# Kernel tuning notes

Measured on AMD Instinct MI355X. Metric: run time of the kernel, lower is better.

Reference implementation:

```python
import jax, jax.numpy as jnp
import numpy as np

N_HEAD = 16
N_KV_HEAD = 4
HEAD_DIM = 128
N_EMBD = 2048
ROPE_BASE = 100000.0
EPS = 1e-6
MASK_VAL = -10000.0


def _rope_tables(t, dtype):
    half = HEAD_DIM // 2
    inv_freq = 1.0 / (ROPE_BASE ** (jnp.arange(half, dtype=jnp.float32) / half))
    freqs = jnp.arange(t, dtype=jnp.float32)[:, None] * inv_freq[None, :]  # [t, half]
    return jnp.cos(freqs).astype(dtype), jnp.sin(freqs).astype(dtype)


def _apply_rope(x, cos, sin):
    # x: [b, t, h, d]; cos/sin: [t, d//2]
    x1, x2 = jnp.split(x, 2, axis=-1)
    c = cos[None, :, None, :]
    s = sin[None, :, None, :]
    return jnp.concatenate([x1 * c + x2 * s, -x1 * s + x2 * c], axis=-1)


def _rms_norm(x):
    return x * jax.lax.rsqrt(jnp.mean(jnp.square(x), axis=-1, keepdims=True) + EPS)


def setup_inputs() -> dict:
    key = jax.random.key(0)
    ks = jax.random.split(key, 5)
    b, t = 2, 2048
    std = 0.02
    return {
        "x": jax.random.normal(ks[0], (b, t, N_EMBD), dtype=jnp.float32),
        "wq": jax.random.normal(ks[1], (N_EMBD, N_HEAD * HEAD_DIM), dtype=jnp.float32) * std,
        "wk": jax.random.normal(ks[2], (N_EMBD, N_KV_HEAD * HEAD_DIM), dtype=jnp.float32) * std,
        "wv": jax.random.normal(ks[3], (N_EMBD, N_KV_HEAD * HEAD_DIM), dtype=jnp.float32) * std,
        "wo": jax.random.normal(ks[4], (N_EMBD, N_EMBD), dtype=jnp.float32) * std,
    }


def reference(x, wq, wk, wv, wo):
    b, t, _ = x.shape
    group = N_HEAD // N_KV_HEAD

    q = (x @ wq).reshape(b, t, N_HEAD, HEAD_DIM)
    k = (x @ wk).reshape(b, t, N_KV_HEAD, HEAD_DIM)
    v = (x @ wv).reshape(b, t, N_KV_HEAD, HEAD_DIM)

    cos, sin = _rope_tables(t, x.dtype)
    q = _rms_norm(_apply_rope(q, cos, sin))
    k = _rms_norm(_apply_rope(k, cos, sin))

    # GQA expand: [b,t,kvh,d] -> [b,t,h,d]
    k = jnp.repeat(k, group, axis=2)
    v = jnp.repeat(v, group, axis=2)

    scale = jax.lax.rsqrt(jnp.asarray(HEAD_DIM, dtype=q.dtype))
    scores = jnp.einsum("bqhd,bkhd->bhqk", q, k) * scale  # [b,h,t,t]

    causal = jnp.tril(jnp.ones((t, t), dtype=bool))
    scores = jnp.where(causal[None, None, :, :], scores, jnp.asarray(MASK_VAL, scores.dtype))

    probs = jax.nn.softmax(scores.astype(jnp.float32), axis=-1).astype(scores.dtype)

    y = jnp.einsum("bhqk,bkhd->bqhd", probs, v).reshape(b, t, N_EMBD)
    return y @ wo
```

## Files before the change

kernel.cpp:

```cpp
#include <hip/hip_runtime.h>
#include <stdint.h>

typedef unsigned short u16;
typedef unsigned int   u32;
typedef float f32x4  __attribute__((ext_vector_type(4)));
typedef float f32x16 __attribute__((ext_vector_type(16)));
typedef short s16x8  __attribute__((ext_vector_type(8)));

#define T_SEQ 2048
#define NE    2048
#define NH    16
#define NKV   4
#define HD    128
#define QKVW  3072

__device__ __forceinline__ u16 f2bf(float f){
  u32 u = __float_as_uint(f);
  u32 r = u + 0x7FFFu + ((u >> 16) & 1u);
  return (u16)(r >> 16);
}
__device__ __forceinline__ float bf2f(u16 h){ return __uint_as_float(((u32)h) << 16); }

__device__ __forceinline__ u32 pkbf(float a, float b){
  u32 r; asm("v_cvt_pk_bf16_f32 %0, %1, %2" : "=v"(r) : "v"(a), "v"(b)); return r;
}

typedef __attribute__((address_space(3))) u32 lds_u32;
typedef __attribute__((address_space(1))) u32 glb_u32;
__device__ __forceinline__ void g2lds16(const void* g, void* l){
  __builtin_amdgcn_global_load_lds((const glb_u32*)g, (lds_u32*)l, 16, 0, 0);
}

#define PREP_NBLK 18944
__global__ __launch_bounds__(256) void k_prep(const float* __restrict__ x,
                                              const float* __restrict__ wq, const float* __restrict__ wk,
                                              const float* __restrict__ wv, const float* __restrict__ wo,
                                              u16* __restrict__ xb, u16* __restrict__ wqkvT, u16* __restrict__ woT,
                                              float* __restrict__ cosT, float* __restrict__ sinT){
  __shared__ float t[32][33];
  const int blk = blockIdx.x, tid = threadIdx.x;
  if (blk < 8192){
    int i = (blk * 256 + tid) * 4;
    float4 v = *(const float4*)(x + i);
    ushort4 o; o.x = f2bf(v.x); o.y = f2bf(v.y); o.z = f2bf(v.z); o.w = f2bf(v.w);
    *(ushort4*)(xb + i) = o;
    return;
  }
  if (blk >= 18432){
    int i = (blk - 18432) * 256 + tid;
    int tt = i >> 6, j = i & 63;
    float inv = expf(-(float)j * (11.512925464970229f / 64.0f));
    float f = (float)tt * inv;
    cosT[i] = cosf(f);
    sinT[i] = sinf(f);
    return;
  }
  const float* in; u16* out; int C; int tt;
  if      (blk < 12288){ in = wq; out = wqkvT;                     C = 2048; tt = blk - 8192;  }
  else if (blk < 13312){ in = wk; out = wqkvT + (size_t)2048*2048; C = 512;  tt = blk - 12288; }
  else if (blk < 14336){ in = wv; out = wqkvT + (size_t)2560*2048; C = 512;  tt = blk - 13312; }
  else                 { in = wo; out = woT;                       C = 2048; tt = blk - 14336; }
  const int r0 = (tt & 63) * 32, c0 = (tt >> 6) * 32;
  const int tx = tid & 31, ty = tid >> 5;
  #pragma unroll
  for (int i = 0; i < 4; ++i) t[ty + i*8][tx] = in[(size_t)(r0 + ty + i*8) * C + c0 + tx];
  __syncthreads();
  #pragma unroll
  for (int i = 0; i < 4; ++i) out[(size_t)(c0 + ty + i*8) * 2048 + r0 + tx] = f2bf(t[tx][ty + i*8]);
}

#define POST_NBLK 22528
__global__ __launch_bounds__(256) void k_post(u16* __restrict__ qkv, u16* __restrict__ vtb,
                                              const float* __restrict__ cosT, const float* __restrict__ sinT,
                                              float qscale){
  __shared__ u16 tsh[32][33];
  const int blk = blockIdx.x, tid = threadIdx.x;
  if (blk < 20480){
    u16* base; int log2h; float scale; int rh;
    if (blk < 16384){ base = qkv;        log2h = 4; scale = qscale; rh = blk * 4 + (tid >> 6); }
    else            { base = qkv + 2048; log2h = 2; scale = 1.0f;   rh = (blk - 16384) * 4 + (tid >> 6); }
    const int lane = tid & 63;
    const int row = rh >> log2h;
    const int h   = rh & ((1 << log2h) - 1);
    const int t   = row & (T_SEQ - 1);
    u16* p = base + (size_t)row * QKVW + h * HD;
    float x1 = bf2f(p[lane]), x2 = bf2f(p[lane + 64]);
    float c = cosT[t * 64 + lane], s = sinT[t * 64 + lane];
    float y1 = x1 * c + x2 * s;
    float y2 = x2 * c - x1 * s;
    float sq = y1 * y1 + y2 * y2;
    #pragma unroll
    for (int off = 32; off; off >>= 1) sq += __shfl_xor(sq, off);
    float sc = rsqrtf(sq * (1.0f / 128.0f) + 1e-6f) * scale;
    p[lane]      = f2bf(y1 * sc);
    p[lane + 64] = f2bf(y2 * sc);
    return;
  }
  const int tt = blk - 20480;
  const int r0 = (tt & 63) * 32, c0 = ((tt >> 6) & 15) * 32, b = tt >> 10;
  const u16* ib = qkv + (size_t)b * T_SEQ * QKVW + 2560;
  u16*       ob = vtb + (size_t)b * 512 * T_SEQ;
  const int tx = tid & 31, ty = tid >> 5;
  #pragma unroll
  for (int i = 0; i < 4; ++i) tsh[ty + i*8][tx] = ib[(size_t)(r0 + ty + i*8) * QKVW + c0 + tx];
  __syncthreads();
  #pragma unroll
  for (int i = 0; i < 4; ++i) ob[(size_t)(c0 + ty + i*8) * T_SEQ + r0 + tx] = tsh[tx][ty + i*8];
}

__device__ __forceinline__ void cstore(u16* C, size_t i, float v){ C[i] = f2bf(v); }
__device__ __forceinline__ void cstore(float* C, size_t i, float v){ C[i] = v; }

template <typename CT>
__global__ __launch_bounds__(256) void k_gemm(const u16* __restrict__ A, const u16* __restrict__ BT,
                                              CT* __restrict__ C, int M, int N, int K, int NPX){
  __shared__ u16 As[128 * 32];
  __shared__ u16 Bs[128 * 32];
  const int tid  = threadIdx.x;
  const int lane = tid & 63;
  const int wid  = tid >> 6;
  const int wr = wid >> 1, wc = wid & 1;
  const int bid = blockIdx.x;
  const int xcd = bid & 7, i = bid >> 3;
  const int ntile = xcd * NPX + i % NPX;
  const int mtile = i / NPX;
  const int tm0 = mtile * 128, tn0 = ntile * 128;
  const int rA   = wid * 32 + (lane >> 2);
  const int kkst = (lane & 3) * 8;
  f32x4 acc[4][4] = {};
  const int nkt = K >> 5;
  for (int kt = 0; kt < nkt; ++kt){
    const int k0 = kt * 32;
    const u16* gA = A  + (size_t)(tm0 + rA) * K + k0 + kkst;
    const u16* gB = BT + (size_t)(tn0 + rA) * K + k0 + kkst;
    g2lds16(gA,            &As[wid * 1024]);
    g2lds16(gA + 16 * K,   &As[wid * 1024 + 512]);
    g2lds16(gB,            &Bs[wid * 1024]);
    g2lds16(gB + 16 * K,   &Bs[wid * 1024 + 512]);
    __syncthreads();
    s16x8 af[4], bfr[4];
    #pragma unroll
    for (int m = 0; m < 4; ++m)
      af[m] = *(const s16x8*)&As[(wr * 64 + m * 16 + (lane & 15)) * 32 + (lane >> 4) * 8];
    #pragma unroll
    for (int n = 0; n < 4; ++n)
      bfr[n] = *(const s16x8*)&Bs[(wc * 64 + n * 16 + (lane & 15)) * 32 + (lane >> 4) * 8];
    #pragma unroll
    for (int m = 0; m < 4; ++m)
      #pragma unroll
      for (int n = 0; n < 4; ++n)
        acc[m][n] = __builtin_amdgcn_mfma_f32_16x16x32_bf16(af[m], bfr[n], acc[m][n], 0, 0, 0);
    __syncthreads();
  }
  #pragma unroll
  for (int m = 0; m < 4; ++m){
    const int row0 = tm0 + wr * 64 + m * 16 + ((lane >> 4) << 2);
    #pragma unroll
    for (int n = 0; n < 4; ++n){
      const int col = tn0 + wc * 64 + n * 16 + (lane & 15);
      #pragma unroll
      for (int r = 0; r < 4; ++r)
        cstore(C, (size_t)(row0 + r) * N + col, acc[m][n][r]);
    }
  }
}

__device__ __forceinline__ s16x8 ldsK(const u16* base, int row, int colB){
  int a = row * 256 + colB; a ^= (row & 7) << 4;
  return *(const s16x8*)((const char*)base + a);
}
__device__ __forceinline__ s16x8 ldsV(const u16* base, int row, int colB){
  int a = row * 128 + colB; a ^= (row & 7) << 4;
  return *(const s16x8*)((const char*)base + a);
}

__global__ __launch_bounds__(512, 2) void k_attn(const u16* __restrict__ qkv, const u16* __restrict__ vt,
                                                 u16* __restrict__ yb){
  __shared__ u16 Kt[2][64 * 128];
  __shared__ u16 Vt[128 * 64];
  const int tid = threadIdx.x, lane = tid & 63, w = tid >> 6;
  const int ql = lane & 31, hi = lane >> 5;

  const int bx = blockIdx.x;
  const int linear = (bx & 7) * 32 + (bx >> 3);
  const int p   = linear & 7;
  const int hl  = (linear >> 3) & 3;
  const int kvh = (linear >> 5) & 3;
  const int b   = (linear >> 7) & 1;
  const int h   = kvh * 4 + hl;

  const int tile = (w < 4) ? (15 - p) : p;
  const int tq0  = tile * 128 + (w & 3) * 32;
  const int myq  = tq0 + ql;
  const int nkb  = 2 * (15 - p) + 2;

  const u16* kg  = qkv + (size_t)(b * T_SEQ) * QKVW + 2048 + kvh * 128;
  const u16* vgb = vt + ((size_t)(b * 512 + kvh * 128)) * T_SEQ;

  auto stageK = [&](int kbI, u16* dst){
    const int ks = kbI * 64;
    #pragma unroll
    for (int cc = 0; cc < 2; ++cc){
      const int call = w * 2 + cc;
      const int o = call * 64 + lane;
      const int f = o ^ ((o >> 4) & 7);
      g2lds16(kg + (size_t)(ks + (o >> 4)) * QKVW + (f & 15) * 8, dst + call * 512);
    }
  };
  auto stageV = [&](int kbI){
    const int ks = kbI * 64;
    #pragma unroll
    for (int cc = 0; cc < 2; ++cc){
      const int call = w * 2 + cc;
      const int o = call * 64 + lane;
      const int f = o ^ ((o >> 3) & 7);
      g2lds16(vgb + (size_t)(o >> 3) * T_SEQ + ks + (f & 7) * 8, Vt + call * 512);
    }
  };

  stageK(0, Kt[0]);

  const u16* qrow = qkv + ((size_t)(b * T_SEQ + myq)) * QKVW + h * HD + hi * 8;
  s16x8 qf[8];
  #pragma unroll
  for (int kc = 0; kc < 8; ++kc) qf[kc] = *(const s16x8*)(qrow + kc * 16);

  f32x16 O[4] = {};
  float mloc = -1e30f, lloc = 0.0f;
  int cur = 0;

  for (int kbI = 0; kbI < nkb; ++kbI){
    const int ks = kbI * 64;

    asm volatile("s_waitcnt vmcnt(0)" ::: "memory");
    __builtin_amdgcn_s_barrier();

    stageV(kbI);
    if (kbI + 1 < nkb) stageK(kbI + 1, Kt[cur ^ 1]);

    int nkc = 0;
    u32 bw[16];
    if (ks <= tq0 + 31){
      const u16* Kc = Kt[cur];
      const bool doN1 = (ks + 32 <= tq0 + 31);
      f32x16 S0 = {}, S1 = {};
      __builtin_amdgcn_s_setprio(1);
      #pragma unroll
      for (int kc = 0; kc < 8; ++kc)
        S0 = __builtin_amdgcn_mfma_f32_32x32x16_bf16(ldsK(Kc, ql, kc*32 + hi*16), qf[kc], S0, 0, 0, 0);
      if (doN1){
        #pragma unroll
        for (int kc = 0; kc < 8; ++kc)
          S1 = __builtin_amdgcn_mfma_f32_32x32x16_bf16(ldsK(Kc, 32 + ql, kc*32 + hi*16), qf[kc], S1, 0, 0, 0);
      }
      __builtin_amdgcn_s_setprio(0);
      if (ks + 31 > tq0){
        #pragma unroll
        for (int r = 0; r < 16; ++r)
          if (ks + (r&3) + 8*(r>>2) + 4*hi > myq) S0[r] = -1e30f;
      }
      if (doN1 && (ks + 63 > tq0)){
        #pragma unroll
        for (int r = 0; r < 16; ++r)
          if (ks + 32 + (r&3) + 8*(r>>2) + 4*hi > myq) S1[r] = -1e30f;
      }
      float mr = -1e30f;
      #pragma unroll
      for (int r = 0; r < 16; ++r) mr = fmaxf(mr, S0[r]);
      if (doN1){
        #pragma unroll
        for (int r = 0; r < 16; ++r) mr = fmaxf(mr, S1[r]);
      }
      mr = fmaxf(mr, __shfl_xor(mr, 32));
      if (!__all(mr <= mloc + 8.0f)){
        const float mn = fmaxf(mloc, mr);
        const float a  = __expf(mloc - mn);
        mloc = mn; lloc *= a;
        #pragma unroll
        for (int dt = 0; dt < 4; ++dt)
          #pragma unroll
          for (int r = 0; r < 16; ++r) O[dt][r] *= a;
      }
      float rs = 0.0f;
      #pragma unroll
      for (int r = 0; r < 16; ++r){ S0[r] = __expf(S0[r] - mloc); rs += S0[r]; }
      if (doN1){
        #pragma unroll
        for (int r = 0; r < 16; ++r){ S1[r] = __expf(S1[r] - mloc); rs += S1[r]; }
      }
      rs += __shfl_xor(rs, 32);
      lloc += rs;
      {
        u32 pk[8], pp[8];
        #pragma unroll
        for (int j = 0; j < 8; ++j) pk[j] = pkbf(S0[2*j], S0[2*j+1]);
        #pragma unroll
        for (int j = 0; j < 8; ++j) pp[j] = (u32)__shfl_xor((int)pk[j], 32);
        bw[0] = hi ? pp[2] : pk[0];  bw[1] = hi ? pp[3] : pk[1];
        bw[2] = hi ? pk[2] : pp[0];  bw[3] = hi ? pk[3] : pp[1];
        bw[4] = hi ? pp[6] : pk[4];  bw[5] = hi ? pp[7] : pk[5];
        bw[6] = hi ? pk[6] : pp[4];  bw[7] = hi ? pk[7] : pp[5];
      }
      nkc = 2;
      if (doN1){
        u32 pk[8], pp[8];
        #pragma unroll
        for (int j = 0; j < 8; ++j) pk[j] = pkbf(S1[2*j], S1[2*j+1]);
        #pragma unroll
        for (int j = 0; j < 8; ++j) pp[j] = (u32)__shfl_xor((int)pk[j], 32);
        bw[8]  = hi ? pp[2] : pk[0];  bw[9]  = hi ? pp[3] : pk[1];
        bw[10] = hi ? pk[2] : pp[0];  bw[11] = hi ? pk[3] : pp[1];
        bw[12] = hi ? pp[6] : pk[4];  bw[13] = hi ? pp[7] : pk[5];
        bw[14] = hi ? pk[6] : pp[4];  bw[15] = hi ? pk[7] : pp[5];
        nkc = 4;
      }
    }

    if (kbI + 1 < nkb) asm volatile("s_waitcnt vmcnt(2)" ::: "memory");
    else               asm volatile("s_waitcnt vmcnt(0)" ::: "memory");
    __builtin_amdgcn_s_barrier();

    __builtin_amdgcn_s_setprio(1);
    #pragma unroll
    for (int kc = 0; kc < 4; ++kc){
      if (kc < nkc){
        union { u32 u[4]; s16x8 v; } pb;
        pb.u[0] = bw[kc*4+0]; pb.u[1] = bw[kc*4+1]; pb.u[2] = bw[kc*4+2]; pb.u[3] = bw[kc*4+3];
        #pragma unroll
        for (int dt = 0; dt < 4; ++dt)
          O[dt] = __builtin_amdgcn_mfma_f32_32x32x16_bf16(ldsV(Vt, dt*32 + ql, kc*32 + hi*16), pb.v, O[dt], 0, 0, 0);
      }
    }
    __builtin_amdgcn_s_setprio(0);
    cur ^= 1;
  }

  const float linv = 1.0f / lloc;
  u16* yr = yb + ((size_t)(b * T_SEQ + myq)) * NE + h * HD;
  #pragma unroll
  for (int dt = 0; dt < 4; ++dt){
    #pragma unroll
    for (int mq = 0; mq < 4; ++mq){
      uint2 s;
      s.x = pkbf(O[dt][4*mq+0] * linv, O[dt][4*mq+1] * linv);
      s.y = pkbf(O[dt][4*mq+2] * linv, O[dt][4*mq+3] * linv);
      *(uint2*)(yr + dt*32 + 8*mq + 4*hi) = s;
    }
  }
}

extern "C" void kernel_launch(void* const* d_in, const int* in_sizes, int n_in,
                              void* d_out, int out_size, void* d_ws, size_t ws_size,
                              hipStream_t stream){
  const float* x  = (const float*)d_in[0];
  const float* wq = (const float*)d_in[1];
  const float* wk = (const float*)d_in[2];
  const float* wv = (const float*)d_in[3];
  const float* wo = (const float*)d_in[4];
  float* out = (float*)d_out;

  char* w = (char*)d_ws;
  u16* xb    = (u16*)w;  w += (size_t)4096 * 2048 * 2;
  u16* wqkvT = (u16*)w;  w += (size_t)3072 * 2048 * 2;
  u16* woT   = (u16*)w;  w += (size_t)2048 * 2048 * 2;
  u16* qkv   = (u16*)w;  w += (size_t)4096 * 3072 * 2;
  u16* vtb   = (u16*)w;  w += (size_t)4096 * 512  * 2;
  u16* yb    = (u16*)w;  w += (size_t)4096 * 2048 * 2;
  float* cosT = (float*)w; w += (size_t)2048 * 64 * 4;
  float* sinT = (float*)w; w += (size_t)2048 * 64 * 4;

  const float SCALE = 0.08838834764831845f;

  k_prep<<<PREP_NBLK, 256, 0, stream>>>(x, wq, wk, wv, wo, xb, wqkvT, woT, cosT, sinT);

  k_gemm<u16><<<768, 256, 0, stream>>>(xb, wqkvT, qkv, 4096, QKVW, 2048, 3);

  k_post<<<POST_NBLK, 256, 0, stream>>>(qkv, vtb, cosT, sinT, SCALE);

  k_attn<<<256, 512, 0, stream>>>(qkv, vtb, yb);

  k_gemm<float><<<512, 256, 0, stream>>>(yb, woT, out, 4096, 2048, 2048, 2);
}
```

Baseline: 236.2 us.

## Triple-buffer GEMM LDS stages with swizzled layout and async prefetch

Reworks the bf16 GEMM main loop into a three-slot LDS ring. Global-to-LDS loads for the next k-halves are issued while MFMAs run on the current slot, with vmcnt-based waits replacing the two full syncthreads per iteration. It also adds an XOR-swizzled LDS layout to cut bank conflicts on fragment reads, raises MFMA wave priority, and sets launch bounds for 3 blocks per CU. The cost is more LDS per block (48KB), which may limit occupancy, plus correctness hinging on precise vmcnt accounting.

```diff
diff --git a/kernel.cpp b/kernel.cpp
--- a/kernel.cpp
+++ b/kernel.cpp
@@ -111,47 +111,108 @@
 __device__ __forceinline__ void cstore(u16* C, size_t i, float v){ C[i] = f2bf(v); }
 __device__ __forceinline__ void cstore(float* C, size_t i, float v){ C[i] = v; }
 
+__device__ __forceinline__ void stage_half(const u16* __restrict__ G, int row0, int K, int k0,
+                                           u16* lds, int w, int lane){
+  #pragma unroll
+  for (int call = 0; call < 2; ++call){
+    const int o  = call * 256 + w * 64 + lane;
+    const int rp = o >> 3, sl = o & 7;
+    const int lg = sl ^ (rp & 7);
+    const int row = rp * 2 + (lg >> 2);
+    const int kc  = lg & 3;
+    g2lds16(G + (size_t)(row0 + row) * K + k0 + kc * 8, lds + (size_t)(call * 256 + w * 64) * 8);
+  }
+}
+
+__device__ __forceinline__ s16x8 ldsFrag(const u16* slotBase, int row, int kchunk){
+  const int byte = (row >> 1) * 128 + (((((row & 1) << 2) | kchunk) ^ ((row >> 1) & 7)) << 4);
+  return *(const s16x8*)((const char*)slotBase + byte);
+}
+
 template <typename CT>
-__global__ __launch_bounds__(256) void k_gemm(const u16* __restrict__ A, const u16* __restrict__ BT,
-                                              CT* __restrict__ C, int M, int N, int K, int NPX){
-  __shared__ u16 As[128 * 32];
-  __shared__ u16 Bs[128 * 32];
+__global__ __launch_bounds__(256, 3) void k_gemm(const u16* __restrict__ A, const u16* __restrict__ BT,
+                                                 CT* __restrict__ C, int M, int N, int K, int NPX){
+  __shared__ u16 As[3 * 4096];
+  __shared__ u16 Bs[3 * 4096];
   const int tid  = threadIdx.x;
   const int lane = tid & 63;
-  const int wid  = tid >> 6;
-  const int wr = wid >> 1, wc = wid & 1;
+  const int w    = tid >> 6;
+  const int wr = w >> 1, wc = w & 1;
   const int bid = blockIdx.x;
-  const int xcd = bid & 7, i = bid >> 3;
-  const int ntile = xcd * NPX + i % NPX;
-  const int mtile = i / NPX;
+  const int xcd = bid & 7, ii = bid >> 3;
+  const int ntile = xcd * NPX + ii % NPX;
+  const int mtile = ii / NPX;
   const int tm0 = mtile * 128, tn0 = ntile * 128;
-  const int rA   = wid * 32 + (lane >> 2);
-  const int kkst = (lane & 3) * 8;
+  const int frow = lane & 15, fk = lane >> 4;
+
   f32x4 acc[4][4] = {};
-  const int nkt = K >> 5;
-  for (int kt = 0; kt < nkt; ++kt){
-    const int k0 = kt * 32;
-    const u16* gA = A  + (size_t)(tm0 + rA) * K + k0 + kkst;
-    const u16* gB = BT + (size_t)(tn0 + rA) * K + k0 + kkst;
-    g2lds16(gA,            &As[wid * 1024]);
-    g2lds16(gA + 16 * K,   &As[wid * 1024 + 512]);
-    g2lds16(gB,            &Bs[wid * 1024]);
-    g2lds16(gB + 16 * K,   &Bs[wid * 1024 + 512]);
-    __syncthreads();
-    s16x8 af[4], bfr[4];
-    #pragma unroll
-    for (int m = 0; m < 4; ++m)
-      af[m] = *(const s16x8*)&As[(wr * 64 + m * 16 + (lane & 15)) * 32 + (lane >> 4) * 8];
-    #pragma unroll
-    for (int n = 0; n < 4; ++n)
-      bfr[n] = *(const s16x8*)&Bs[(wc * 64 + n * 16 + (lane & 15)) * 32 + (lane >> 4) * 8];
-    #pragma unroll
-    for (int m = 0; m < 4; ++m)
-      #pragma unroll
-      for (int n = 0; n < 4; ++n)
-        acc[m][n] = __builtin_amdgcn_mfma_f32_16x16x32_bf16(af[m], bfr[n], acc[m][n], 0, 0, 0);
-    __syncthreads();
-  }
+  const int nkt = K >> 6;
+
+  stage_half(A,  tm0, K, 0,  As,        w, lane);
+  stage_half(BT, tn0, K, 0,  Bs,        w, lane);
+  stage_half(A,  tm0, K, 32, As + 4096, w, lane);
+  stage_half(BT, tn0, K, 32, Bs + 4096, w, lane);
+  asm volatile("s_waitcnt vmcnt(4)" ::: "memory");
+  __builtin_amdgcn_s_barrier();
+
+  int s = 0;
+  #pragma unroll 1
+  for (int t = 0; t < nkt; ++t){
+    const int s1 = (s + 1 > 2) ? 0 : s + 1;
+    const int s2 = (s + 2 > 2) ? s - 1 : s + 2;
+    const bool more = (t + 1 < nkt);
+
+    if (more){
+      stage_half(A,  tm0, K, (t + 1) * 64,  As + s2 * 4096, w, lane);
+      stage_half(BT, tn0, K, (t + 1) * 64,  Bs + s2 * 4096, w, lane);
+    }
+    {
+      const u16* Ap = As + s * 4096;
+      const u16* Bp = Bs + s * 4096;
+      s16x8 af[4], bfr[4];
+      #pragma unroll
+      for (int m = 0; m < 4; ++m) af[m]  = ldsFrag(Ap, wr * 64 + m * 16 + frow, fk);
+      #pragma unroll
+      for (int n = 0; n < 4; ++n) bfr[n] = ldsFrag(Bp, wc * 64 + n * 16 + frow, fk);
+      __builtin_amdgcn_s_setprio(1);
+      #pragma unroll
+      for (int m = 0; m < 4; ++m)
+        #pragma unroll
+        for (int n = 0; n < 4; ++n)
+          acc[m][n] = __builtin_amdgcn_mfma_f32_16x16x32_bf16(af[m], bfr[n], acc[m][n], 0, 0, 0);
+      __builtin_amdgcn_s_setprio(0);
+    }
+    if (more) asm volatile("s_waitcnt vmcnt(4)" ::: "memory");
+    else      asm volatile("s_waitcnt vmcnt(0)" ::: "memory");
+    __builtin_amdgcn_s_barrier();
+
+    if (more){
+      stage_half(A,  tm0, K, (t + 1) * 64 + 32, As + s * 4096, w, lane);
+      stage_half(BT, tn0, K, (t + 1) * 64 + 32, Bs + s * 4096, w, lane);
+    }
+    {
+      const u16* Ap = As + s1 * 4096;
+      const u16* Bp = Bs + s1 * 4096;
+      s16x8 af[4], bfr[4];
+      #pragma unroll
+      for (int m = 0; m < 4; ++m) af[m]  = ldsFrag(Ap, wr * 64 + m * 16 + frow, fk);
+      #pragma unroll
+      for (int n = 0; n < 4; ++n) bfr[n] = ldsFrag(Bp, wc * 64 + n * 16 + frow, fk);
+      __builtin_amdgcn_s_setprio(1);
+      #pragma unroll
+      for (int m = 0; m < 4; ++m)
+        #pragma unroll
+        for (int n = 0; n < 4; ++n)
+          acc[m][n] = __builtin_amdgcn_mfma_f32_16x16x32_bf16(af[m], bfr[n], acc[m][n], 0, 0, 0);
+      __builtin_amdgcn_s_setprio(0);
+    }
+    if (more){
+      asm volatile("s_waitcnt vmcnt(4)" ::: "memory");
+      __builtin_amdgcn_s_barrier();
+    }
+    s = s2;
+  }
+
   #pragma unroll
   for (int m = 0; m < 4; ++m){
     const int row0 = tm0 + wr * 64 + m * 16 + ((lane >> 4) << 2);
```

Result: faster. 222.9 us (-5.6%).
